# Kernel tuning notes

Measured on AMD Instinct MI355X. Metric: run time of the kernel, lower is better.

Reference implementation:

```python
import jax, jax.numpy as jnp
import numpy as np

M, K, N, GROUP = 4096, 4096, 14336, 64


def setup_inputs() -> dict:
    key = jax.random.key(0)
    k1, k2, k3 = jax.random.split(key, 3)
    x = jax.random.normal(k1, (M, K), dtype=jnp.float32)
    # int4 quantized weight values in [0, 15], symmetric around zero-point 8
    q_weight = jax.random.randint(k2, (K, N), 0, 16, dtype=jnp.int32)
    # per-group scales: one scale per GROUP rows of k, per output column
    scales = jax.random.uniform(k3, (K // GROUP, N), dtype=jnp.float32) * 0.02
    return {"x": x, "q_weight": q_weight, "scales": scales, "group_size": GROUP}


def reference(x, q_weight, scales, group_size):
    # Marlin int4 GEMM math (act_order=False): dequantize per k-group, then GEMM.
    k, n = q_weight.shape
    g = k // group_size
    # (q - 8) * scale, scale broadcast over each group of `group_size` k-rows
    w = (q_weight.reshape(g, group_size, n).astype(scales.dtype) - 8.0) * scales[:, None, :]
    w = w.reshape(k, n)  # [K, N] dequantized weight
    return x @ w  # [M, N]
```

## Files before the change

kernel.cpp:

```cpp
#include <hip/hip_runtime.h>

#define MDIM 4096
#define KDIM 4096
#define NDIM 14336

typedef __attribute__((ext_vector_type(8))) short bf16x8;
typedef __attribute__((ext_vector_type(4))) short bf16x4;
typedef __attribute__((ext_vector_type(4))) float f32x4;

__device__ __forceinline__ unsigned short f2bf(float f) {
  unsigned u = __float_as_uint(f);
  return (unsigned short)((u + 0x7FFFu + ((u >> 16) & 1u)) >> 16);
}

__device__ __forceinline__ void async_copy16(const void* g, void* l) {
  __builtin_amdgcn_global_load_lds((const __attribute__((address_space(1))) unsigned*)g,
                                   (__attribute__((address_space(3))) unsigned*)l, 16, 0, 0);
}

__global__ __launch_bounds__(256) void cvt_x_kernel(const float* __restrict__ X,
                                                    short* __restrict__ Xb) {
  const int i = blockIdx.x * 256 + threadIdx.x;
  const float4* p = (const float4*)X + (size_t)i * 2;
  const float4 a = p[0], b = p[1];
  bf16x8 v;
  v[0] = f2bf(a.x); v[1] = f2bf(a.y); v[2] = f2bf(a.z); v[3] = f2bf(a.w);
  v[4] = f2bf(b.x); v[5] = f2bf(b.y); v[6] = f2bf(b.z); v[7] = f2bf(b.w);
  *((bf16x8*)Xb + i) = v;
}

constexpr int DQ_STRIDE = 264;
__global__ __launch_bounds__(512) void dequant_w_kernel(const int* __restrict__ Q,
                                                        const float* __restrict__ S,
                                                        short* __restrict__ Wt) {
  __shared__ short Ls[128 * DQ_STRIDE];
  const int k0 = blockIdx.x * 256;
  const int n0 = blockIdx.y * 128;
  const int t  = threadIdx.x;

  const int n4  = (t & 31) * 4;
  const int rbi = (t >> 5) * 4;
#pragma unroll
  for (int kc = 0; kc < 4; ++kc) {
    const int g  = (k0 >> 6) + kc;
    const int kb = k0 + kc * 64 + rbi;
    const float4 s4 = *(const float4*)(S + (size_t)g * NDIM + n0 + n4);
    int4 q[4];
#pragma unroll
    for (int i = 0; i < 4; ++i)
      q[i] = *(const int4*)(Q + (size_t)(kb + i) * NDIM + n0 + n4);
    short* lp = &Ls[n4 * DQ_STRIDE + kc * 64 + rbi];
    bf16x4 v;
    v[0] = (short)f2bf((float)(q[0].x - 8) * s4.x);
    v[1] = (short)f2bf((float)(q[1].x - 8) * s4.x);
    v[2] = (short)f2bf((float)(q[2].x - 8) * s4.x);
    v[3] = (short)f2bf((float)(q[3].x - 8) * s4.x);
    *(bf16x4*)(lp + 0 * DQ_STRIDE) = v;
    v[0] = (short)f2bf((float)(q[0].y - 8) * s4.y);
    v[1] = (short)f2bf((float)(q[1].y - 8) * s4.y);
    v[2] = (short)f2bf((float)(q[2].y - 8) * s4.y);
    v[3] = (short)f2bf((float)(q[3].y - 8) * s4.y);
    *(bf16x4*)(lp + 1 * DQ_STRIDE) = v;
    v[0] = (short)f2bf((float)(q[0].z - 8) * s4.z);
    v[1] = (short)f2bf((float)(q[1].z - 8) * s4.z);
    v[2] = (short)f2bf((float)(q[2].z - 8) * s4.z);
    v[3] = (short)f2bf((float)(q[3].z - 8) * s4.z);
    *(bf16x4*)(lp + 2 * DQ_STRIDE) = v;
    v[0] = (short)f2bf((float)(q[0].w - 8) * s4.w);
    v[1] = (short)f2bf((float)(q[1].w - 8) * s4.w);
    v[2] = (short)f2bf((float)(q[2].w - 8) * s4.w);
    v[3] = (short)f2bf((float)(q[3].w - 8) * s4.w);
    *(bf16x4*)(lp + 3 * DQ_STRIDE) = v;
  }
  __syncthreads();

  const int c = (t & 7) * 8;
#pragma unroll
  for (int p = 0; p < 2; ++p) {
    const int nr = (t >> 3) + p * 64;
    const short* lr = &Ls[nr * DQ_STRIDE + c];
    short* wp = Wt + (size_t)(n0 + nr) * KDIM + k0 + c;
#pragma unroll
    for (int r = 0; r < 4; ++r)
      *(bf16x8*)(wp + r * 64) = *(const bf16x8*)(lr + r * 64);
  }
}

__global__ __launch_bounds__(256, 2)
void gemm_bf16tt(const short* __restrict__ Xb, const short* __restrict__ Wt,
                 float* __restrict__ Out) {
  __shared__ short As[128 * 64];
  __shared__ short Bs[128 * 64];

  const int bm = blockIdx.x * 128;
  const int bn = blockIdx.y * 128;
  const int tid = threadIdx.x, lane = tid & 63, wave = tid >> 6;
  const int wm = (wave & 1) * 64, wn = (wave >> 1) * 64;
  const int quad = lane >> 4, l16 = lane & 15;
  const int lx = l16 & 7;

  f32x4 acc[4][4];
#pragma unroll
  for (int i = 0; i < 4; ++i)
#pragma unroll
    for (int j = 0; j < 4; ++j) acc[i][j] = (f32x4){0.f, 0.f, 0.f, 0.f};

  const int row0 = tid >> 3;
  const int kof  = (((tid & 7) ^ (row0 & 7))) * 8;
  const size_t aoff = (size_t)(bm + row0) * KDIM + kof;
  const size_t boff = (size_t)(bn + row0) * KDIM + kof;
  short* const la = &As[(wave * 64) * 8];
  short* const lb = &Bs[(wave * 64) * 8];

  for (int kt = 0; kt < KDIM / 64; ++kt) {
    const int k0 = kt * 64;
    __syncthreads();
#pragma unroll
    for (int p = 0; p < 4; ++p) {
      async_copy16(Xb + aoff + (size_t)p * 32 * KDIM + k0, la + p * 2048);
      async_copy16(Wt + boff + (size_t)p * 32 * KDIM + k0, lb + p * 2048);
    }
    __syncthreads();

#pragma unroll
    for (int kk = 0; kk < 64; kk += 32) {
      const int sbase = kk >> 3;
      bf16x8 af[4], bfr[4];
#pragma unroll
      for (int i = 0; i < 4; ++i)
        af[i] = *(const bf16x8*)&As[(wm + i * 16 + l16) * 64 + (((sbase + quad) ^ lx) << 3)];
#pragma unroll
      for (int j = 0; j < 4; ++j)
        bfr[j] = *(const bf16x8*)&Bs[(wn + j * 16 + l16) * 64 + (((sbase + quad) ^ lx) << 3)];
#pragma unroll
      for (int i = 0; i < 4; ++i)
#pragma unroll
        for (int j = 0; j < 4; ++j)
          acc[i][j] = __builtin_amdgcn_mfma_f32_16x16x32_bf16(af[i], bfr[j], acc[i][j], 0, 0, 0);
    }
  }

#pragma unroll
  for (int i = 0; i < 4; ++i) {
    const int r0 = bm + wm + i * 16 + quad * 4;
#pragma unroll
    for (int j = 0; j < 4; ++j) {
      const int col = bn + wn + j * 16 + l16;
#pragma unroll
      for (int r = 0; r < 4; ++r)
        Out[(size_t)(r0 + r) * NDIM + col] = acc[i][j][r];
    }
  }
}

constexpr int BKP = 72;
__global__ __launch_bounds__(256, 2)
void marlin_int4_gemm(const float* __restrict__ X, const int* __restrict__ Q,
                      const float* __restrict__ S, float* __restrict__ Out) {
  __shared__ short As[128 * BKP];
  __shared__ short Bs[128 * BKP];
  const int bm = blockIdx.x * 128, bn = blockIdx.y * 128;
  const int tid = threadIdx.x, lane = tid & 63, wave = tid >> 6;
  const int wm = (wave & 1) * 64, wn = (wave >> 1) * 64;
  const int quad = lane >> 4, l16 = lane & 15;
  const int nB = tid & 127, krB = (tid >> 7) * 32;
  f32x4 acc[4][4];
#pragma unroll
  for (int i = 0; i < 4; ++i)
#pragma unroll
    for (int j = 0; j < 4; ++j) acc[i][j] = (f32x4){0.f, 0.f, 0.f, 0.f};
  for (int kt = 0; kt < KDIM / 64; ++kt) {
    const int k0 = kt * 64;
    const float s = S[kt * NDIM + bn + nB];
    const float bias = -8.0f * s;
    __syncthreads();
#pragma unroll
    for (int i = 0; i < 8; ++i) {
      const int idx4 = tid + (i << 8);
      const int row = idx4 >> 4, col = (idx4 & 15) << 2;
      const float4 v = *(const float4*)(X + (size_t)(bm + row) * KDIM + k0 + col);
      ushort4 b;
      b.x = f2bf(v.x); b.y = f2bf(v.y); b.z = f2bf(v.z); b.w = f2bf(v.w);
      *(ushort4*)(&As[row * BKP + col]) = b;
    }
    unsigned short wb[32];
#pragma unroll
    for (int j = 0; j < 32; ++j) {
      const int qv = Q[(size_t)(k0 + krB + j) * NDIM + bn + nB];
      wb[j] = f2bf((float)qv * s + bias);
    }
    {
      short* brow = &Bs[nB * BKP + krB];
#pragma unroll
      for (int c = 0; c < 4; ++c) {
        bf16x8 v;
#pragma unroll
        for (int e = 0; e < 8; ++e) v[e] = (short)wb[c * 8 + e];
        *(bf16x8*)(brow + c * 8) = v;
      }
    }
    __syncthreads();
#pragma unroll
    for (int kk = 0; kk < 64; kk += 32) {
      bf16x8 af[4], bfr[4];
#pragma unroll
      for (int i = 0; i < 4; ++i)
        af[i] = *(const bf16x8*)&As[(wm + i * 16 + l16) * BKP + kk + quad * 8];
#pragma unroll
      for (int j = 0; j < 4; ++j)
        bfr[j] = *(const bf16x8*)&Bs[(wn + j * 16 + l16) * BKP + kk + quad * 8];
#pragma unroll
      for (int i = 0; i < 4; ++i)
#pragma unroll
        for (int j = 0; j < 4; ++j)
          acc[i][j] = __builtin_amdgcn_mfma_f32_16x16x32_bf16(af[i], bfr[j], acc[i][j], 0, 0, 0);
    }
  }
#pragma unroll
  for (int i = 0; i < 4; ++i) {
    const int r0 = bm + wm + i * 16 + quad * 4;
#pragma unroll
    for (int j = 0; j < 4; ++j) {
      const int col = bn + wn + j * 16 + l16;
#pragma unroll
      for (int r = 0; r < 4; ++r)
        Out[(size_t)(r0 + r) * NDIM + col] = acc[i][j][r];
    }
  }
}

extern "C" void kernel_launch(void* const* d_in, const int* in_sizes, int n_in,
                              void* d_out, int out_size, void* d_ws, size_t ws_size,
                              hipStream_t stream) {
  const float* X = (const float*)d_in[0];
  const int*   Q = (const int*)d_in[1];
  const float* S = (const float*)d_in[2];
  float* Out = (float*)d_out;

  const size_t xb_elems = (size_t)MDIM * KDIM;
  const size_t wt_elems = (size_t)NDIM * KDIM;
  const size_t need = (xb_elems + wt_elems) * sizeof(short);

  if (ws_size >= need) {
    short* Xb = (short*)d_ws;
    short* Wt = Xb + xb_elems;
    cvt_x_kernel<<<(int)(xb_elems / 8 / 256), 256, 0, stream>>>(X, Xb);
    dequant_w_kernel<<<dim3(KDIM / 256, NDIM / 128), 512, 0, stream>>>(Q, S, Wt);
    gemm_bf16tt<<<dim3(MDIM / 128, NDIM / 128), 256, 0, stream>>>(Xb, Wt, Out);
  } else {
    marlin_int4_gemm<<<dim3(MDIM / 128, NDIM / 128), 256, 0, stream>>>(X, Q, S, Out);
  }
}
```

Baseline: 852.2 us.

## Use 32x32x16 bf16 MFMA and swizzle block order in GEMM

New measurement: 954.7 us. +12.0%, slower.

```diff
diff --git a/kernel.cpp b/kernel.cpp
--- a/kernel.cpp
+++ b/kernel.cpp
@@ -7,6 +7,7 @@
 typedef __attribute__((ext_vector_type(8))) short bf16x8;
 typedef __attribute__((ext_vector_type(4))) short bf16x4;
 typedef __attribute__((ext_vector_type(4))) float f32x4;
+typedef __attribute__((ext_vector_type(16))) float f32x16;
 
 __device__ __forceinline__ unsigned short f2bf(float f) {
   unsigned u = __float_as_uint(f);
@@ -92,18 +93,23 @@
   __shared__ short As[128 * 64];
   __shared__ short Bs[128 * 64];
 
-  const int bm = blockIdx.x * 128;
-  const int bn = blockIdx.y * 128;
+  const int lin = blockIdx.y * gridDim.x + blockIdx.x;
+  const int swz = (lin & 7) * 448 + (lin >> 3);
+  const int bm = (swz & 31) * 128;
+  const int bn = (swz >> 5) * 128;
+
   const int tid = threadIdx.x, lane = tid & 63, wave = tid >> 6;
   const int wm = (wave & 1) * 64, wn = (wave >> 1) * 64;
-  const int quad = lane >> 4, l16 = lane & 15;
-  const int lx = l16 & 7;
-
-  f32x4 acc[4][4];
-#pragma unroll
-  for (int i = 0; i < 4; ++i)
-#pragma unroll
-    for (int j = 0; j < 4; ++j) acc[i][j] = (f32x4){0.f, 0.f, 0.f, 0.f};
+  const int l32 = lane & 31, khalf = lane >> 5;
+  const int lx = l32 & 7;
+
+  f32x16 acc[2][2];
+#pragma unroll
+  for (int i = 0; i < 2; ++i)
+#pragma unroll
+    for (int j = 0; j < 2; ++j)
+#pragma unroll
+      for (int r = 0; r < 16; ++r) acc[i][j][r] = 0.f;
 
   const int row0 = tid >> 3;
   const int kof  = (((tid & 7) ^ (row0 & 7))) * 8;
@@ -123,32 +129,34 @@
     __syncthreads();
 
 #pragma unroll
-    for (int kk = 0; kk < 64; kk += 32) {
-      const int sbase = kk >> 3;
-      bf16x8 af[4], bfr[4];
-#pragma unroll
-      for (int i = 0; i < 4; ++i)
-        af[i] = *(const bf16x8*)&As[(wm + i * 16 + l16) * 64 + (((sbase + quad) ^ lx) << 3)];
-#pragma unroll
-      for (int j = 0; j < 4; ++j)
-        bfr[j] = *(const bf16x8*)&Bs[(wn + j * 16 + l16) * 64 + (((sbase + quad) ^ lx) << 3)];
-#pragma unroll
-      for (int i = 0; i < 4; ++i)
-#pragma unroll
-        for (int j = 0; j < 4; ++j)
-          acc[i][j] = __builtin_amdgcn_mfma_f32_16x16x32_bf16(af[i], bfr[j], acc[i][j], 0, 0, 0);
-    }
-  }
-
-#pragma unroll
-  for (int i = 0; i < 4; ++i) {
-    const int r0 = bm + wm + i * 16 + quad * 4;
-#pragma unroll
-    for (int j = 0; j < 4; ++j) {
-      const int col = bn + wn + j * 16 + l16;
-#pragma unroll
-      for (int r = 0; r < 4; ++r)
-        Out[(size_t)(r0 + r) * NDIM + col] = acc[i][j][r];
+    for (int kk = 0; kk < 64; kk += 16) {
+      const int ch = (kk >> 3) + khalf;
+      const int sl = (ch ^ lx) << 3;
+      bf16x8 af[2], bfr[2];
+#pragma unroll
+      for (int i = 0; i < 2; ++i)
+        af[i] = *(const bf16x8*)&As[(wm + i * 32 + l32) * 64 + sl];
+#pragma unroll
+      for (int j = 0; j < 2; ++j)
+        bfr[j] = *(const bf16x8*)&Bs[(wn + j * 32 + l32) * 64 + sl];
+#pragma unroll
+      for (int i = 0; i < 2; ++i)
+#pragma unroll
+        for (int j = 0; j < 2; ++j)
+          acc[i][j] = __builtin_amdgcn_mfma_f32_32x32x16_bf16(af[i], bfr[j], acc[i][j], 0, 0, 0);
+    }
+  }
+
+#pragma unroll
+  for (int i = 0; i < 2; ++i) {
+#pragma unroll
+    for (int j = 0; j < 2; ++j) {
+      const int col = bn + wn + j * 32 + l32;
+#pragma unroll
+      for (int r = 0; r < 16; ++r) {
+        const int row = bm + wm + i * 32 + (r & 3) + 8 * (r >> 2) + 4 * khalf;
+        Out[(size_t)row * NDIM + col] = acc[i][j][r];
+      }
     }
   }
 }
```

## Use 256x256 tiles with double-buffered LDS and interleaved async prefetch in bf16 GEMM

Applied to the files above, without the earlier changes.

New measurement: 880.5 us. 3.3% more time.

```diff
diff --git a/kernel.cpp b/kernel.cpp
--- a/kernel.cpp
+++ b/kernel.cpp
@@ -16,6 +16,13 @@
 __device__ __forceinline__ void async_copy16(const void* g, void* l) {
   __builtin_amdgcn_global_load_lds((const __attribute__((address_space(1))) unsigned*)g,
                                    (__attribute__((address_space(3))) unsigned*)l, 16, 0, 0);
+}
+
+__device__ __forceinline__ bf16x8 ds_read_b128(const short* p) {
+  bf16x8 r;
+  auto lp = (const __attribute__((address_space(3))) short*)p;
+  asm volatile("ds_read_b128 %0, %1" : "=v"(r) : "v"(lp));
+  return r;
 }
 
 __global__ __launch_bounds__(256) void cvt_x_kernel(const float* __restrict__ X,
@@ -86,66 +93,99 @@
   }
 }
 
-__global__ __launch_bounds__(256, 2)
+__global__ __launch_bounds__(512, 1)
 void gemm_bf16tt(const short* __restrict__ Xb, const short* __restrict__ Wt,
                  float* __restrict__ Out) {
-  __shared__ short As[128 * 64];
-  __shared__ short Bs[128 * 64];
-
-  const int bm = blockIdx.x * 128;
-  const int bn = blockIdx.y * 128;
+  __shared__ short As[2][256 * 64];
+  __shared__ short Bs[2][256 * 64];
+
+  const int bm = blockIdx.x * 256;
+  const int bn = blockIdx.y * 256;
   const int tid = threadIdx.x, lane = tid & 63, wave = tid >> 6;
-  const int wm = (wave & 1) * 64, wn = (wave >> 1) * 64;
+  const int wr = wave >> 2;
+  const int wc = wave & 3;
   const int quad = lane >> 4, l16 = lane & 15;
   const int lx = l16 & 7;
 
-  f32x4 acc[4][4];
-#pragma unroll
-  for (int i = 0; i < 4; ++i)
+  f32x4 acc[8][4];
+#pragma unroll
+  for (int i = 0; i < 8; ++i)
 #pragma unroll
     for (int j = 0; j < 4; ++j) acc[i][j] = (f32x4){0.f, 0.f, 0.f, 0.f};
 
   const int row0 = tid >> 3;
-  const int kof  = (((tid & 7) ^ (row0 & 7))) * 8;
+  const int kof  = ((tid & 7) ^ (row0 & 7)) * 8;
   const size_t aoff = (size_t)(bm + row0) * KDIM + kof;
   const size_t boff = (size_t)(bn + row0) * KDIM + kof;
-  short* const la = &As[(wave * 64) * 8];
-  short* const lb = &Bs[(wave * 64) * 8];
-
-  for (int kt = 0; kt < KDIM / 64; ++kt) {
-    const int k0 = kt * 64;
-    __syncthreads();
-#pragma unroll
-    for (int p = 0; p < 4; ++p) {
-      async_copy16(Xb + aoff + (size_t)p * 32 * KDIM + k0, la + p * 2048);
-      async_copy16(Wt + boff + (size_t)p * 32 * KDIM + k0, lb + p * 2048);
-    }
-    __syncthreads();
-
-#pragma unroll
-    for (int kk = 0; kk < 64; kk += 32) {
-      const int sbase = kk >> 3;
-      bf16x8 af[4], bfr[4];
-#pragma unroll
-      for (int i = 0; i < 4; ++i)
-        af[i] = *(const bf16x8*)&As[(wm + i * 16 + l16) * 64 + (((sbase + quad) ^ lx) << 3)];
-#pragma unroll
-      for (int j = 0; j < 4; ++j)
-        bfr[j] = *(const bf16x8*)&Bs[(wn + j * 16 + l16) * 64 + (((sbase + quad) ^ lx) << 3)];
-#pragma unroll
-      for (int i = 0; i < 4; ++i)
-#pragma unroll
-        for (int j = 0; j < 4; ++j)
-          acc[i][j] = __builtin_amdgcn_mfma_f32_16x16x32_bf16(af[i], bfr[j], acc[i][j], 0, 0, 0);
-    }
-  }
-
-#pragma unroll
-  for (int i = 0; i < 4; ++i) {
-    const int r0 = bm + wm + i * 16 + quad * 4;
+  const int ldst_off = wave * 8 * 64;
+
+#define STAGE_G(buf, g, kt1)                                                          \
+  do {                                                                                \
+    const short* gsrc = (((g) < 2) ? (Xb + aoff) : (Wt + boff)) +                     \
+                        (size_t)((g) & 1) * 128 * KDIM + (size_t)(kt1) * 64;          \
+    short* ldst = (((g) < 2) ? As[buf] : Bs[buf]) + (((g) & 1) * 128) * 64 + ldst_off;\
+    async_copy16(gsrc, ldst);                                                         \
+    async_copy16(gsrc + (size_t)64 * KDIM, ldst + 64 * 64);                           \
+  } while (0)
+
+#define PHASE_COMPUTE(cur, mh, nh)                                                    \
+  do {                                                                                \
+    const short* Ab = As[cur];                                                        \
+    const short* Bb = Bs[cur];                                                        \
+    bf16x8 af[4][2], bv[2][2];                                                        \
+    _Pragma("unroll") for (int s = 0; s < 2; ++s) {                                   \
+      const int sl = (((s * 4 + quad)) ^ lx) << 3;                                    \
+      _Pragma("unroll") for (int i = 0; i < 4; ++i)                                   \
+        af[i][s] = ds_read_b128(&Ab[(wr * 128 + ((mh) * 4 + i) * 16 + l16) * 64 + sl]);\
+      _Pragma("unroll") for (int j = 0; j < 2; ++j)                                   \
+        bv[j][s] = ds_read_b128(&Bb[(wc * 64 + ((nh) * 2 + j) * 16 + l16) * 64 + sl]);\
+    }                                                                                 \
+    asm volatile("s_waitcnt lgkmcnt(0)" ::: "memory");                                \
+    __builtin_amdgcn_sched_barrier(0);                                                \
+    __builtin_amdgcn_s_setprio(1);                                                    \
+    _Pragma("unroll") for (int i = 0; i < 4; ++i)                                     \
+      _Pragma("unroll") for (int j = 0; j < 2; ++j)                                   \
+        _Pragma("unroll") for (int s = 0; s < 2; ++s)                                 \
+          acc[(mh) * 4 + i][(nh) * 2 + j] = __builtin_amdgcn_mfma_f32_16x16x32_bf16(  \
+              af[i][s], bv[j][s], acc[(mh) * 4 + i][(nh) * 2 + j], 0, 0, 0);          \
+    __builtin_amdgcn_s_setprio(0);                                                    \
+  } while (0)
+
+  constexpr int NT = KDIM / 64;
+
+#pragma unroll
+  for (int g = 0; g < 4; ++g) STAGE_G(0, g, 0);
+
+  for (int kt = 0; kt < NT; ++kt) {
+    const int cur = kt & 1, nxt = cur ^ 1;
+    const bool pre = (kt + 1 < NT);
+    __builtin_amdgcn_s_barrier();
+    __builtin_amdgcn_sched_barrier(0);
+    if (pre) {
+      STAGE_G(nxt, 0, kt + 1);
+      asm volatile("s_waitcnt vmcnt(2)" ::: "memory");
+    } else {
+      asm volatile("s_waitcnt vmcnt(0)" ::: "memory");
+    }
+    __builtin_amdgcn_s_barrier();
+    __builtin_amdgcn_sched_barrier(0);
+    PHASE_COMPUTE(cur, 0, 0);
+    if (pre) STAGE_G(nxt, 1, kt + 1);
+    PHASE_COMPUTE(cur, 0, 1);
+    if (pre) STAGE_G(nxt, 2, kt + 1);
+    PHASE_COMPUTE(cur, 1, 0);
+    if (pre) STAGE_G(nxt, 3, kt + 1);
+    PHASE_COMPUTE(cur, 1, 1);
+  }
+#undef STAGE_G
+#undef PHASE_COMPUTE
+
+#pragma unroll
+  for (int i = 0; i < 8; ++i) {
+    const int r0 = bm + wr * 128 + i * 16 + quad * 4;
 #pragma unroll
     for (int j = 0; j < 4; ++j) {
-      const int col = bn + wn + j * 16 + l16;
+      const int col = bn + wc * 64 + j * 16 + l16;
 #pragma unroll
       for (int r = 0; r < 4; ++r)
         Out[(size_t)(r0 + r) * NDIM + col] = acc[i][j][r];
@@ -246,7 +286,7 @@
     short* Wt = Xb + xb_elems;
     cvt_x_kernel<<<(int)(xb_elems / 8 / 256), 256, 0, stream>>>(X, Xb);
     dequant_w_kernel<<<dim3(KDIM / 256, NDIM / 128), 512, 0, stream>>>(Q, S, Wt);
-    gemm_bf16tt<<<dim3(MDIM / 128, NDIM / 128), 256, 0, stream>>>(Xb, Wt, Out);
+    gemm_bf16tt<<<dim3(MDIM / 256, NDIM / 256), 512, 0, stream>>>(Xb, Wt, Out);
   } else {
     marlin_int4_gemm<<<dim3(MDIM / 128, NDIM / 128), 256, 0, stream>>>(X, Q, S, Out);
   }
```
